# Kernel optimization log

Measured on AMD Instinct MI355X. Metric: run time of the kernel, lower is better.

## Reference

```python
import jax, jax.numpy as jnp
import numpy as np

R = 32            # voxel resolution
DIM = 240         # channels C
EPS_NORM = 0.0    # module eps
BN_EPS = 1e-5     # torch BatchNorm1d default eps


def setup_inputs() -> dict:
    key = jax.random.key(0)
    k1, k2, k3 = jax.random.split(key, 3)
    B, C, N = 4, DIM, 32768
    features = jax.random.normal(k1, (B, C, N), jnp.float32)
    coords = jax.random.uniform(k2, (B, 3, N), jnp.float32)
    # mlp params: Conv1d(2C -> C, kernel 1) + BatchNorm1d(C)
    w = jax.random.normal(k3, (C, 2 * C), jnp.float32) / np.sqrt(2 * C).astype(np.float32)
    b = jnp.zeros((C,), jnp.float32)
    gamma = jnp.ones((C,), jnp.float32)
    beta = jnp.zeros((C,), jnp.float32)
    return {"features": features, "coords": coords, "w": w, "b": b, "gamma": gamma, "beta": beta}


def _voxelize(features, coords):
    # normalize coords into [0, 1], scale to voxel grid
    nc = coords - coords.mean(axis=2, keepdims=True)                      # [B,3,N]
    scale = jnp.linalg.norm(nc, axis=1, keepdims=True).max(axis=2, keepdims=True) * 2.0 + EPS_NORM
    nc = nc / scale + 0.5
    nc = jnp.clip(nc * R, 0, R - 1)
    vox = jnp.round(nc).astype(jnp.int32)
    pos = vox[:, 0] + vox[:, 1] * R + vox[:, 2] * (R * R)                 # [B,N] flattened voxel id
    R3 = R * R * R

    def per_batch(f, p):
        # f: [C,N], p: [N] -> [2C, R3]; per-voxel max feature + second (min) feature
        mx = jax.ops.segment_max(f.T, p, num_segments=R3)                 # [R3, C]
        mn = jax.ops.segment_min(f.T, p, num_segments=R3)                 # [R3, C]
        cnt = jax.ops.segment_sum(jnp.ones_like(p), p, num_segments=R3)  # [R3]
        mask = (cnt > 0)[:, None]
        mx = jnp.where(mask, mx, 0.0)
        mn = jnp.where(mask, mn, 0.0)
        return jnp.concatenate([mx, mn], axis=1).T                        # [2C, R3]

    fea = jax.vmap(per_batch)(features, pos)                              # [B,2C,R3]
    return fea, nc


def reference(features, coords, w, b, gamma, beta):
    fea, nc = _voxelize(features, coords)
    # 1x1 Conv1d (pointwise GEMM) + BatchNorm1d (training-mode batch stats) + Swish
    y = jnp.einsum('co,bov->bcv', w, fea) + b[None, :, None]
    mean = y.mean(axis=(0, 2), keepdims=True)
    var = y.var(axis=(0, 2), keepdims=True)
    y = gamma[None, :, None] * (y - mean) * jax.lax.rsqrt(var + BN_EPS) + beta[None, :, None]
    y = y * jax.nn.sigmoid(y)
    B, C, _ = features.shape
    return y.reshape(B, C, R, R, R), nc
```

## Files before the change

kernel.cpp:

```cpp
#include <hip/hip_runtime.h>
#include <cstdint>
#include <cstddef>

#define RR 32
#define R3 32768
#define NPT 32768
#define CH 240
#define CH2 480
#define NB 4
#define NTILES 2048
#define Y_ELEMS 31457280

typedef __attribute__((ext_vector_type(8))) short short8v;
typedef __attribute__((ext_vector_type(4))) float float4v;

union u8pack { short8v v; unsigned short u[8]; };

static __device__ __forceinline__ float bf2f(unsigned short u) {
  return __uint_as_float(((unsigned int)u) << 16);
}
static __device__ __forceinline__ unsigned short f2bf(float f) {
  unsigned int u = __float_as_uint(f);
  u = (u + 0x7FFFu + ((u >> 16) & 1u)) >> 16;
  return (unsigned short)u;
}

__global__ void k_init(int* __restrict__ cnt, float* __restrict__ stats,
                       const float* __restrict__ w, unsigned short* __restrict__ wfrag,
                       int* __restrict__ tilectr) {
  int g = blockIdx.x * 256 + threadIdx.x;
  if (g == 0) *tilectr = 0;
  if (g < NB * R3) cnt[g] = 0;
  if (g < 4096) stats[g] = 0.0f;
  if (g < 14400) {
    int lane = g & 63, t = g >> 6;
    int mg = t / 75, r = t % 75;
    int kc = r / 5, mL = r % 5;
    int m = mg * 5 + mL;
    int ln = lane & 15, q = lane >> 4;
    const float* src = w + (size_t)(m * 16 + ln) * CH2 + kc * 32 + q * 8;
    u8pack pk;
#pragma unroll
    for (int j = 0; j < 8; j++) pk.u[j] = f2bf(src[j]);
    *(short8v*)&wfrag[(size_t)g * 8] = pk.v;
  }
}

__global__ __launch_bounds__(1024) void k_coord_stats(const float* __restrict__ coords,
                                                      float* __restrict__ ms) {
  __shared__ float red[1024];
  __shared__ float mean[3];
  int b = blockIdx.x, t = threadIdx.x;
  const float4* cb4 = (const float4*)(coords + (size_t)b * 3 * NPT);
  float s[3] = {0.f, 0.f, 0.f};
  for (int i = t; i < NPT / 4; i += 1024) {
#pragma unroll
    for (int d = 0; d < 3; d++) {
      float4 v = cb4[d * (NPT / 4) + i];
      s[d] += (v.x + v.y) + (v.z + v.w);
    }
  }
  for (int d = 0; d < 3; d++) {
    red[t] = s[d]; __syncthreads();
    for (int k = 512; k > 0; k >>= 1) { if (t < k) red[t] += red[t + k]; __syncthreads(); }
    if (t == 0) mean[d] = red[0] * (1.0f / NPT);
    __syncthreads();
  }
  float m0 = mean[0], m1 = mean[1], m2 = mean[2];
  float mx = 0.f;
  for (int i = t; i < NPT / 4; i += 1024) {
    float4 x = cb4[i], y = cb4[NPT / 4 + i], z = cb4[2 * (NPT / 4) + i];
    float dx, dy, dz, n;
    dx = x.x - m0; dy = y.x - m1; dz = z.x - m2; n = dx * dx + dy * dy + dz * dz; mx = fmaxf(mx, n);
    dx = x.y - m0; dy = y.y - m1; dz = z.y - m2; n = dx * dx + dy * dy + dz * dz; mx = fmaxf(mx, n);
    dx = x.z - m0; dy = y.z - m1; dz = z.z - m2; n = dx * dx + dy * dy + dz * dz; mx = fmaxf(mx, n);
    dx = x.w - m0; dy = y.w - m1; dz = z.w - m2; n = dx * dx + dy * dy + dz * dz; mx = fmaxf(mx, n);
  }
  red[t] = mx; __syncthreads();
  for (int k = 512; k > 0; k >>= 1) { if (t < k) red[t] = fmaxf(red[t], red[t + k]); __syncthreads(); }
  if (t == 0) {
    ms[b * 4 + 0] = m0; ms[b * 4 + 1] = m1; ms[b * 4 + 2] = m2;
    ms[b * 4 + 3] = sqrtf(red[0]) * 2.0f;
  }
}

__global__ void k_pos_nc(const float* __restrict__ coords, const float* __restrict__ ms,
                         float* __restrict__ ncout, int* __restrict__ pos, int* __restrict__ cnt) {
  int g = blockIdx.x * 256 + threadIdx.x;
  int b = g >> 15, i = g & (NPT - 1);
  const float* cb = coords + (size_t)b * 3 * NPT;
  float scale = ms[b * 4 + 3];
  int vox[3];
#pragma unroll
  for (int d = 0; d < 3; d++) {
    float v = (cb[(size_t)d * NPT + i] - ms[b * 4 + d]) / scale + 0.5f;
    v = fminf(fmaxf(v * (float)RR, 0.0f), (float)(RR - 1));
    ncout[((size_t)(b * 3 + d)) * NPT + i] = v;
    vox[d] = (int)rintf(v);
  }
  int p = (b << 15) | (vox[0] + (vox[1] << 5) + (vox[2] << 10));
  pos[g] = p;
  atomicAdd(&cnt[p], 1);
}

__global__ void k_scan(const int* __restrict__ cnt, int* __restrict__ offs) {
  __shared__ int part[1024];
  int b = blockIdx.x, t = threadIdx.x;
  const int base = b * R3;
  int local[32];
  int s = 0;
#pragma unroll
  for (int j = 0; j < 32; j++) { local[j] = cnt[base + t * 32 + j]; s += local[j]; }
  part[t] = s; __syncthreads();
  for (int d = 1; d < 1024; d <<= 1) {
    int v = (t >= d) ? part[t - d] : 0;
    __syncthreads();
    part[t] += v;
    __syncthreads();
  }
  int run = (t == 0) ? 0 : part[t - 1];
#pragma unroll
  for (int j = 0; j < 32; j++) { offs[base + t * 32 + j] = run; run += local[j]; }
}

__global__ void k_scatter(const int* __restrict__ pos, int* __restrict__ offs,
                          int* __restrict__ rank) {
  int g = blockIdx.x * 256 + threadIdx.x;
  int p = pos[g];
  int slot = atomicAdd(&offs[p], 1);
  rank[g] = slot;
}

__global__ void k_transpose3(const float* __restrict__ f, const int* __restrict__ rank,
                             unsigned short* __restrict__ fts) {
  __shared__ float tile[CH * 65];
  __shared__ int slts[64];
  int p0 = blockIdx.x * 64, b = blockIdx.y;
  int t = threadIdx.x;
  if (t < 64) slts[t] = rank[b * NPT + p0 + t];
  {
    int pp = t & 63, cq = t >> 6;
    const float* src = f + ((size_t)b * CH) * NPT + p0 + pp;
#pragma unroll 4
    for (int j = 0; j < 60; ++j) {
      int c = j * 4 + cq;
      tile[c * 65 + pp] = src[(size_t)c * NPT];
    }
  }
  __syncthreads();
  int ch8 = t & 7;
#pragma unroll
  for (int pass = 0; pass < 2; ++pass) {
    int p = pass * 32 + (t >> 3);
    unsigned short* dst = fts + ((size_t)(b * NPT + slts[p])) * CH;
#pragma unroll
    for (int i = 0; i < 4; ++i) {
      int ch = ch8 + 8 * i;
      if (ch < 30) {
        u8pack pk;
#pragma unroll
        for (int jj = 0; jj < 8; ++jj) pk.u[jj] = f2bf(tile[(ch * 8 + jj) * 65 + p]);
        *(short8v*)&dst[ch * 8] = pk.v;
      }
    }
  }
}

__global__ __launch_bounds__(512, 4) void k_fused(const int* __restrict__ cnt,
                                                  const int* __restrict__ offs,
                                                  const unsigned short* __restrict__ fts,
                                                  const unsigned short* __restrict__ wfrag,
                                                  const float* __restrict__ bias,
                                                  unsigned short* __restrict__ ybf,
                                                  float* __restrict__ gstats,
                                                  int* __restrict__ tilectr) {
  __shared__ unsigned short fB[4 * 15 * 512];
  __shared__ int scnt[64], soffs[64], vlist[64];
  __shared__ int qh, qm, tilebuf[2];
  int tid = threadIdx.x;
  int wave = tid >> 6, lane = tid & 63;
  int sub = lane >> 5, l = lane & 31;
  int ln = lane & 15, q = lane >> 4;

  int t1c = 30 + l;
  int kc0 = l >> 2, q0 = l & 3;
  int kc1 = t1c >> 2, q1 = t1c & 3;

  int nmt = (wave == 7) ? 1 : 2;
  int mt0 = wave * 2, mt1 = wave * 2 + (nmt - 1);
  const unsigned short* wp0 = wfrag + ((size_t)((mt0 / 5) * 75 + (mt0 % 5)) * 512) + lane * 8;
  const unsigned short* wp1 = wfrag + ((size_t)((mt1 / 5) * 75 + (mt1 % 5)) * 512) + lane * 8;

  float bb[2][4];
#pragma unroll
  for (int mm = 0; mm < 2; ++mm) {
    int mt = (mm == 0) ? mt0 : mt1;
#pragma unroll
    for (int r = 0; r < 4; ++r) bb[mm][r] = bias[mt * 16 + q * 4 + r];
  }
  float sacc[2][4], sqacc[2][4];
#pragma unroll
  for (int mm = 0; mm < 2; ++mm)
#pragma unroll
    for (int r = 0; r < 4; ++r) { sacc[mm][r] = 0.f; sqacc[mm][r] = 0.f; }

  int par = 0;
  if (tid == 0) tilebuf[0] = atomicAdd(tilectr, 1);

  while (true) {
    __syncthreads();
    int T = tilebuf[par];
    if (T >= NTILES) break;
    int b = T >> 9;
    int bbase = b << 15;
    int v0 = (T & 511) * 64;

    {
      int4 z4 = {0, 0, 0, 0};
      for (int i = tid; i < 3840; i += 512) ((int4*)fB)[i] = z4;
    }
    if (wave == 0) {
      int n = cnt[T * 64 + lane];
      int st = offs[T * 64 + lane];
      scnt[lane] = n; soffs[lane] = st;
      unsigned long long mask = __ballot(n > 0);
      int pfx = __popcll(mask & ((1ull << lane) - 1ull));
      if (n > 0) vlist[pfx] = lane;
      if (lane == 0) { qm = __popcll(mask); qh = 0; }
    }
    if (tid == 0) tilebuf[par ^ 1] = atomicAdd(tilectr, 1);
    par ^= 1;
    __syncthreads();

    int qmL = qm;
    while (true) {
      int p;
      if (l == 0) p = atomicAdd(&qh, 1);
      p = __shfl(p, sub << 5);
      if (p >= qmL) break;
      int lv = vlist[p];
      int n = scnt[lv];
      int start = soffs[lv] - n;
      int cg = lv >> 4, cc = lv & 15;
      if (l < 30) {
        const unsigned short* sp = fts + (size_t)(bbase + start) * CH + l * 8;
        int lim = (n - 1) * CH;
        float mx[8], mn[8];
#pragma unroll
        for (int k = 0; k < 8; k++) { mx[k] = -__builtin_inff(); mn[k] = __builtin_inff(); }
        for (int j = 0; j < n; j += 8) {
          int base = j * CH;
          u8pack u0, u1, u2, u3, u4, u5, u6, u7;
          int o0 = base;           o0 = o0 < lim ? o0 : lim;
          int o1 = base + CH;      o1 = o1 < lim ? o1 : lim;
          int o2 = base + 2 * CH;  o2 = o2 < lim ? o2 : lim;
          int o3 = base + 3 * CH;  o3 = o3 < lim ? o3 : lim;
          int o4 = base + 4 * CH;  o4 = o4 < lim ? o4 : lim;
          int o5 = base + 5 * CH;  o5 = o5 < lim ? o5 : lim;
          int o6 = base + 6 * CH;  o6 = o6 < lim ? o6 : lim;
          int o7 = base + 7 * CH;  o7 = o7 < lim ? o7 : lim;
          u0.v = *(const short8v*)(sp + o0);
          u1.v = *(const short8v*)(sp + o1);
          u2.v = *(const short8v*)(sp + o2);
          u3.v = *(const short8v*)(sp + o3);
          u4.v = *(const short8v*)(sp + o4);
          u5.v = *(const short8v*)(sp + o5);
          u6.v = *(const short8v*)(sp + o6);
          u7.v = *(const short8v*)(sp + o7);
#pragma unroll
          for (int k = 0; k < 8; k++) {
            float a0 = bf2f(u0.u[k]), a1 = bf2f(u1.u[k]);
            float a2 = bf2f(u2.u[k]), a3 = bf2f(u3.u[k]);
            float a4 = bf2f(u4.u[k]), a5 = bf2f(u5.u[k]);
            float a6 = bf2f(u6.u[k]), a7 = bf2f(u7.u[k]);
            float hx = fmaxf(fmaxf(fmaxf(a0, a1), fmaxf(a2, a3)),
                             fmaxf(fmaxf(a4, a5), fmaxf(a6, a7)));
            float hn = fminf(fminf(fminf(a0, a1), fminf(a2, a3)),
                             fminf(fminf(a4, a5), fminf(a6, a7)));
            mx[k] = fmaxf(mx[k], hx);
            mn[k] = fminf(mn[k], hn);
          }
        }
        u8pack omx, omn;
#pragma unroll
        for (int k = 0; k < 8; k++) { omx.u[k] = f2bf(mx[k]); omn.u[k] = f2bf(mn[k]); }
        int ci0 = (q0 * 16 + cc) ^ (kc0 & 7);
        int ci1 = (q1 * 16 + cc) ^ (kc1 & 7);
        *(short8v*)&fB[((cg * 15 + kc0) * 64 + ci0) * 8] = omx.v;
        *(short8v*)&fB[((cg * 15 + kc1) * 64 + ci1) * 8] = omn.v;
      }
    }
    __syncthreads();

    float4v acc[2][4];
#pragma unroll
    for (int mm = 0; mm < 2; ++mm)
#pragma unroll
      for (int cg = 0; cg < 4; ++cg) acc[mm][cg] = (float4v){0.f, 0.f, 0.f, 0.f};

    short8v w0[2], w1[2];
    w0[0] = *(const short8v*)(wp0);
    w0[1] = *(const short8v*)(wp0 + 5 * 512);
    w1[0] = *(const short8v*)(wp1);
    w1[1] = *(const short8v*)(wp1 + 5 * 512);
#pragma unroll
    for (int kc = 0; kc < 15; ++kc) {
      const unsigned short* fbl = fB + (size_t)((lane ^ (kc & 7)) * 8);
      short8v bfv[4];
#pragma unroll
      for (int cg = 0; cg < 4; ++cg)
        bfv[cg] = *(const short8v*)(fbl + (size_t)(cg * 15 + kc) * 512);
      short8v wn0, wn1;
      if (kc + 2 < 15) {
        wn0 = *(const short8v*)(wp0 + (size_t)(kc + 2) * 5 * 512);
        wn1 = *(const short8v*)(wp1 + (size_t)(kc + 2) * 5 * 512);
      }
#pragma unroll
      for (int cg = 0; cg < 4; ++cg)
        acc[0][cg] = __builtin_amdgcn_mfma_f32_16x16x32_bf16(w0[kc & 1], bfv[cg], acc[0][cg], 0, 0, 0);
      if (nmt > 1)
#pragma unroll
        for (int cg = 0; cg < 4; ++cg)
          acc[1][cg] = __builtin_amdgcn_mfma_f32_16x16x32_bf16(w1[kc & 1], bfv[cg], acc[1][cg], 0, 0, 0);
      if (kc + 2 < 15) { w0[kc & 1] = wn0; w1[kc & 1] = wn1; }
    }

    unsigned short* yb = ybf + ((size_t)b * CH) * R3 + v0 + ln;
#pragma unroll
    for (int mm = 0; mm < 2; ++mm)
      if (mm < nmt) {
        int mt = (mm == 0) ? mt0 : mt1;
#pragma unroll
        for (int r = 0; r < 4; ++r) {
          int c = mt * 16 + q * 4 + r;
          unsigned short* yrow = yb + (size_t)c * R3;
          float bbv = bb[mm][r];
          float s = 0.f, sq = 0.f;
#pragma unroll
          for (int cg = 0; cg < 4; ++cg) {
            float yv = acc[mm][cg][r] + bbv;
            yrow[cg * 16] = f2bf(yv);
            s += yv; sq += yv * yv;
          }
          sacc[mm][r] += s;
          sqacc[mm][r] += sq;
        }
      }
  }

  float* gslot = gstats + (size_t)(blockIdx.x & 7) * 512;
#pragma unroll
  for (int mm = 0; mm < 2; ++mm)
    if (mm < nmt) {
      int mt = (mm == 0) ? mt0 : mt1;
#pragma unroll
      for (int r = 0; r < 4; ++r) {
        float s = sacc[mm][r], sq = sqacc[mm][r];
#pragma unroll
        for (int off = 1; off < 16; off <<= 1) {
          s += __shfl_xor(s, off);
          sq += __shfl_xor(sq, off);
        }
        if (ln == 0) {
          int c = mt * 16 + q * 4 + r;
          atomicAdd(&gslot[c], s);
          atomicAdd(&gslot[256 + c], sq);
        }
      }
    }
}

__global__ void k_apply(const unsigned short* __restrict__ ybf, float* __restrict__ out,
                        const float* __restrict__ stats, const float* __restrict__ gamma,
                        const float* __restrict__ beta) {
  int g = blockIdx.x * 256 + threadIdx.x;
  int c = (g >> 12) % CH;
  const float ninv = 1.0f / (float)(NB * R3);
  float sum = 0.f, ssq = 0.f;
#pragma unroll
  for (int sl = 0; sl < 8; ++sl) {
    sum += stats[sl * 512 + c];
    ssq += stats[sl * 512 + 256 + c];
  }
  float mean = sum * ninv;
  float var = ssq * ninv - mean * mean;
  float s = gamma[c] * rsqrtf(var + 1e-5f);
  float h = beta[c] - mean * s;
  u8pack v;
  v.v = *(const short8v*)(ybf + (size_t)g * 8);
  float4 o0, o1;
  float t;
  t = bf2f(v.u[0]) * s + h; o0.x = t / (1.0f + __expf(-t));
  t = bf2f(v.u[1]) * s + h; o0.y = t / (1.0f + __expf(-t));
  t = bf2f(v.u[2]) * s + h; o0.z = t / (1.0f + __expf(-t));
  t = bf2f(v.u[3]) * s + h; o0.w = t / (1.0f + __expf(-t));
  t = bf2f(v.u[4]) * s + h; o1.x = t / (1.0f + __expf(-t));
  t = bf2f(v.u[5]) * s + h; o1.y = t / (1.0f + __expf(-t));
  t = bf2f(v.u[6]) * s + h; o1.z = t / (1.0f + __expf(-t));
  t = bf2f(v.u[7]) * s + h; o1.w = t / (1.0f + __expf(-t));
  ((float4*)out)[(size_t)g * 2] = o0;
  ((float4*)out)[(size_t)g * 2 + 1] = o1;
}

extern "C" void kernel_launch(void* const* d_in, const int* in_sizes, int n_in,
                              void* d_out, int out_size, void* d_ws, size_t ws_size,
                              hipStream_t stream) {
  const float* features = (const float*)d_in[0];
  const float* coords   = (const float*)d_in[1];
  const float* w        = (const float*)d_in[2];
  const float* bias     = (const float*)d_in[3];
  const float* gamma    = (const float*)d_in[4];
  const float* beta     = (const float*)d_in[5];
  float* out = (float*)d_out;

  char* ws = (char*)d_ws;
  size_t off = 0;
  float* ms    = (float*)(ws + off); off += 256;
  int* tilectr = (int*)(ws + off);   off += 256;
  float* stats = (float*)(ws + off); off += 16384;
  int* pos     = (int*)(ws + off);   off += (size_t)NB * NPT * 4;
  int* cnt     = (int*)(ws + off);   off += (size_t)NB * R3 * 4;
  int* offs    = (int*)(ws + off);   off += (size_t)NB * R3 * 4;
  int* rank    = (int*)(ws + off);   off += (size_t)NB * NPT * 4;
  unsigned short* wfrag = (unsigned short*)(ws + off); off += (size_t)CH * CH2 * 2;
  unsigned short* fts   = (unsigned short*)(ws + off); off += (size_t)NB * NPT * CH * 2;
  unsigned short* ybf   = (unsigned short*)(ws + off); off += (size_t)NB * R3 * CH * 2;

  float* ncout = out + Y_ELEMS;

  k_init<<<516, 256, 0, stream>>>(cnt, stats, w, wfrag, tilectr);
  k_coord_stats<<<4, 1024, 0, stream>>>(coords, ms);
  k_pos_nc<<<512, 256, 0, stream>>>(coords, ms, ncout, pos, cnt);
  k_scan<<<4, 1024, 0, stream>>>(cnt, offs);
  k_scatter<<<512, 256, 0, stream>>>(pos, offs, rank);
  k_transpose3<<<dim3(512, 4), 256, 0, stream>>>(features, rank, fts);
  k_fused<<<512, 512, 0, stream>>>(cnt, offs, fts, wfrag, bias, ybf, stats, tilectr);
  k_apply<<<Y_ELEMS / 2048, 256, 0, stream>>>(ybf, out, stats, gamma, beta);
}
```

Baseline: 430.1 us.

## Software-pipeline voxel gather with MFMA GEMM using double-buffered LDS tiles

Measured after the change: 364.6 us. 1.18x faster.

```diff
diff --git a/kernel.cpp b/kernel.cpp
--- a/kernel.cpp
+++ b/kernel.cpp
@@ -166,7 +166,7 @@
   }
 }
 
-__global__ __launch_bounds__(512, 4) void k_fused(const int* __restrict__ cnt,
+__global__ __launch_bounds__(512, 2) void k_fused(const int* __restrict__ cnt,
                                                   const int* __restrict__ offs,
                                                   const unsigned short* __restrict__ fts,
                                                   const unsigned short* __restrict__ wfrag,
@@ -174,73 +174,57 @@
                                                   unsigned short* __restrict__ ybf,
                                                   float* __restrict__ gstats,
                                                   int* __restrict__ tilectr) {
-  __shared__ unsigned short fB[4 * 15 * 512];
-  __shared__ int scnt[64], soffs[64], vlist[64];
-  __shared__ int qh, qm, tilebuf[2];
+  __shared__ unsigned short fB[2][4 * 15 * 512];
+  __shared__ int scnt[2][64], soffs[2][64], vlist[2][64];
+  __shared__ int qh[2], qm[2], tq[4];
   int tid = threadIdx.x;
   int wave = tid >> 6, lane = tid & 63;
   int sub = lane >> 5, l = lane & 31;
   int ln = lane & 15, q = lane >> 4;
 
+  int nmt = (wave == 7) ? 1 : 2;
+  short8v wreg[2][15];
+#pragma unroll
+  for (int mm = 0; mm < 2; ++mm)
+    if (mm < nmt) {
+      int mt = wave * 2 + mm;
+      int mg = mt / 5, mL = mt % 5;
+      const unsigned short* wp = wfrag + ((size_t)(mg * 75 + mL) * 512) + lane * 8;
+#pragma unroll
+      for (int kc = 0; kc < 15; ++kc)
+        wreg[mm][kc] = *(const short8v*)(wp + (size_t)kc * 5 * 512);
+    }
+
+  float bb[2][4];
+#pragma unroll
+  for (int mm = 0; mm < 2; ++mm)
+    if (mm < nmt) {
+      int mt = wave * 2 + mm;
+#pragma unroll
+      for (int r = 0; r < 4; ++r) bb[mm][r] = bias[mt * 16 + q * 4 + r];
+    }
+  float sacc[2][4], sqacc[2][4];
+#pragma unroll
+  for (int mm = 0; mm < 2; ++mm)
+#pragma unroll
+    for (int r = 0; r < 4; ++r) { sacc[mm][r] = 0.f; sqacc[mm][r] = 0.f; }
+
   int t1c = 30 + l;
   int kc0 = l >> 2, q0 = l & 3;
   int kc1 = t1c >> 2, q1 = t1c & 3;
 
-  int nmt = (wave == 7) ? 1 : 2;
-  int mt0 = wave * 2, mt1 = wave * 2 + (nmt - 1);
-  const unsigned short* wp0 = wfrag + ((size_t)((mt0 / 5) * 75 + (mt0 % 5)) * 512) + lane * 8;
-  const unsigned short* wp1 = wfrag + ((size_t)((mt1 / 5) * 75 + (mt1 % 5)) * 512) + lane * 8;
-
-  float bb[2][4];
-#pragma unroll
-  for (int mm = 0; mm < 2; ++mm) {
-    int mt = (mm == 0) ? mt0 : mt1;
-#pragma unroll
-    for (int r = 0; r < 4; ++r) bb[mm][r] = bias[mt * 16 + q * 4 + r];
-  }
-  float sacc[2][4], sqacc[2][4];
-#pragma unroll
-  for (int mm = 0; mm < 2; ++mm)
-#pragma unroll
-    for (int r = 0; r < 4; ++r) { sacc[mm][r] = 0.f; sqacc[mm][r] = 0.f; }
-
-  int par = 0;
-  if (tid == 0) tilebuf[0] = atomicAdd(tilectr, 1);
-
-  while (true) {
-    __syncthreads();
-    int T = tilebuf[par];
-    if (T >= NTILES) break;
-    int b = T >> 9;
-    int bbase = b << 15;
-    int v0 = (T & 511) * 64;
-
-    {
-      int4 z4 = {0, 0, 0, 0};
-      for (int i = tid; i < 3840; i += 512) ((int4*)fB)[i] = z4;
-    }
-    if (wave == 0) {
-      int n = cnt[T * 64 + lane];
-      int st = offs[T * 64 + lane];
-      scnt[lane] = n; soffs[lane] = st;
-      unsigned long long mask = __ballot(n > 0);
-      int pfx = __popcll(mask & ((1ull << lane) - 1ull));
-      if (n > 0) vlist[pfx] = lane;
-      if (lane == 0) { qm = __popcll(mask); qh = 0; }
-    }
-    if (tid == 0) tilebuf[par ^ 1] = atomicAdd(tilectr, 1);
-    par ^= 1;
-    __syncthreads();
-
-    int qmL = qm;
+  auto GATHER = [&](int sb, int T) {
+    unsigned short* fb = fB[sb];
+    int bbase = (T >> 9) << 15;
+    int qmL = qm[sb];
     while (true) {
       int p;
-      if (l == 0) p = atomicAdd(&qh, 1);
+      if (l == 0) p = atomicAdd(&qh[sb], 1);
       p = __shfl(p, sub << 5);
       if (p >= qmL) break;
-      int lv = vlist[p];
-      int n = scnt[lv];
-      int start = soffs[lv] - n;
+      int lv = vlist[sb][p];
+      int n = scnt[sb][lv];
+      int start = soffs[sb][lv] - n;
       int cg = lv >> 4, cc = lv & 15;
       if (l < 30) {
         const unsigned short* sp = fts + (size_t)(bbase + start) * CH + l * 8;
@@ -286,11 +270,69 @@
         for (int k = 0; k < 8; k++) { omx.u[k] = f2bf(mx[k]); omn.u[k] = f2bf(mn[k]); }
         int ci0 = (q0 * 16 + cc) ^ (kc0 & 7);
         int ci1 = (q1 * 16 + cc) ^ (kc1 & 7);
-        *(short8v*)&fB[((cg * 15 + kc0) * 64 + ci0) * 8] = omx.v;
-        *(short8v*)&fB[((cg * 15 + kc1) * 64 + ci1) * 8] = omn.v;
+        *(short8v*)&fb[((cg * 15 + kc0) * 64 + ci0) * 8] = omx.v;
+        *(short8v*)&fb[((cg * 15 + kc1) * 64 + ci1) * 8] = omn.v;
       }
     }
+  };
+
+  if (wave == 0) {
+    int t;
+    if (lane == 0) t = atomicAdd(tilectr, 1);
+    int T0w = __shfl(t, 0);
+    if (lane == 0) t = atomicAdd(tilectr, 1);
+    int T1w = __shfl(t, 0);
+    if (lane == 0) { tq[0] = T0w; tq[1] = T1w; }
+    int na = 0, oa = 0, nb2 = 0, ob = 0;
+    if (T0w < NTILES) { na = cnt[T0w * 64 + lane]; oa = offs[T0w * 64 + lane]; }
+    if (T1w < NTILES) { nb2 = cnt[T1w * 64 + lane]; ob = offs[T1w * 64 + lane]; }
+    scnt[0][lane] = na; soffs[0][lane] = oa;
+    {
+      unsigned long long m = __ballot(na > 0);
+      int pfx = __popcll(m & ((1ull << lane) - 1ull));
+      if (na > 0) vlist[0][pfx] = lane;
+      if (lane == 0) { qm[0] = __popcll(m); qh[0] = 0; }
+    }
+    scnt[1][lane] = nb2; soffs[1][lane] = ob;
+    {
+      unsigned long long m = __ballot(nb2 > 0);
+      int pfx = __popcll(m & ((1ull << lane) - 1ull));
+      if (nb2 > 0) vlist[1][pfx] = lane;
+      if (lane == 0) { qm[1] = __popcll(m); qh[1] = 0; }
+    }
+  }
+  {
+    int4 z4 = {0, 0, 0, 0};
+    for (int i2 = tid; i2 < 3840; i2 += 512) ((int4*)fB[0])[i2] = z4;
+  }
+  __syncthreads();
+  {
+    int T0v = tq[0];
+    if (T0v < NTILES) GATHER(0, T0v);
+  }
+
+  for (int it = 0;; ++it) {
     __syncthreads();
+    int T = tq[it & 3];
+    if (T >= NTILES) break;
+    int cb = it & 1, nb = cb ^ 1;
+    int Tn = tq[(it + 1) & 3];
+
+    {
+      int4 z4 = {0, 0, 0, 0};
+      for (int i2 = tid; i2 < 3840; i2 += 512) ((int4*)fB[nb])[i2] = z4;
+    }
+    int n2 = 0, o2 = 0;
+    if (wave == 0) {
+      int t;
+      if (lane == 0) t = atomicAdd(tilectr, 1);
+      int Tn2 = __shfl(t, 0);
+      if (lane == 0) tq[(it + 2) & 3] = Tn2;
+      if (Tn2 < NTILES) { n2 = cnt[Tn2 * 64 + lane]; o2 = offs[Tn2 * 64 + lane]; }
+    }
+    __syncthreads();
+
+    if (Tn < NTILES) GATHER(nb, Tn);
 
     float4v acc[2][4];
 #pragma unroll
@@ -298,38 +340,29 @@
 #pragma unroll
       for (int cg = 0; cg < 4; ++cg) acc[mm][cg] = (float4v){0.f, 0.f, 0.f, 0.f};
 
-    short8v w0[2], w1[2];
-    w0[0] = *(const short8v*)(wp0);
-    w0[1] = *(const short8v*)(wp0 + 5 * 512);
-    w1[0] = *(const short8v*)(wp1);
-    w1[1] = *(const short8v*)(wp1 + 5 * 512);
+    const unsigned short* fbase = fB[cb];
 #pragma unroll
     for (int kc = 0; kc < 15; ++kc) {
-      const unsigned short* fbl = fB + (size_t)((lane ^ (kc & 7)) * 8);
+      const unsigned short* fbl = fbase + (size_t)((lane ^ (kc & 7)) * 8);
       short8v bfv[4];
 #pragma unroll
       for (int cg = 0; cg < 4; ++cg)
         bfv[cg] = *(const short8v*)(fbl + (size_t)(cg * 15 + kc) * 512);
-      short8v wn0, wn1;
-      if (kc + 2 < 15) {
-        wn0 = *(const short8v*)(wp0 + (size_t)(kc + 2) * 5 * 512);
-        wn1 = *(const short8v*)(wp1 + (size_t)(kc + 2) * 5 * 512);
-      }
-#pragma unroll
-      for (int cg = 0; cg < 4; ++cg)
-        acc[0][cg] = __builtin_amdgcn_mfma_f32_16x16x32_bf16(w0[kc & 1], bfv[cg], acc[0][cg], 0, 0, 0);
-      if (nmt > 1)
-#pragma unroll
-        for (int cg = 0; cg < 4; ++cg)
-          acc[1][cg] = __builtin_amdgcn_mfma_f32_16x16x32_bf16(w1[kc & 1], bfv[cg], acc[1][cg], 0, 0, 0);
-      if (kc + 2 < 15) { w0[kc & 1] = wn0; w1[kc & 1] = wn1; }
-    }
-
-    unsigned short* yb = ybf + ((size_t)b * CH) * R3 + v0 + ln;
+#pragma unroll
+      for (int mm = 0; mm < 2; ++mm)
+        if (mm < nmt)
+#pragma unroll
+          for (int cg = 0; cg < 4; ++cg)
+            acc[mm][cg] = __builtin_amdgcn_mfma_f32_16x16x32_bf16(wreg[mm][kc], bfv[cg], acc[mm][cg], 0, 0, 0);
+    }
+
+    int bt = T >> 9;
+    int v0 = (T & 511) * 64;
+    unsigned short* yb = ybf + ((size_t)bt * CH) * R3 + v0 + ln;
 #pragma unroll
     for (int mm = 0; mm < 2; ++mm)
       if (mm < nmt) {
-        int mt = (mm == 0) ? mt0 : mt1;
+        int mt = wave * 2 + mm;
 #pragma unroll
         for (int r = 0; r < 4; ++r) {
           int c = mt * 16 + q * 4 + r;
@@ -346,13 +379,22 @@
           sqacc[mm][r] += sq;
         }
       }
+
+    if (wave == 0) {
+      int s2 = it & 1;
+      scnt[s2][lane] = n2; soffs[s2][lane] = o2;
+      unsigned long long m = __ballot(n2 > 0);
+      int pfx = __popcll(m & ((1ull << lane) - 1ull));
+      if (n2 > 0) vlist[s2][pfx] = lane;
+      if (lane == 0) { qm[s2] = __popcll(m); qh[s2] = 0; }
+    }
   }
 
   float* gslot = gstats + (size_t)(blockIdx.x & 7) * 512;
 #pragma unroll
   for (int mm = 0; mm < 2; ++mm)
     if (mm < nmt) {
-      int mt = (mm == 0) ? mt0 : mt1;
+      int mt = wave * 2 + mm;
 #pragma unroll
       for (int r = 0; r < 4; ++r) {
         float s = sacc[mm][r], sq = sqacc[mm][r];
@@ -434,6 +476,6 @@
   k_scan<<<4, 1024, 0, stream>>>(cnt, offs);
   k_scatter<<<512, 256, 0, stream>>>(pos, offs, rank);
   k_transpose3<<<dim3(512, 4), 256, 0, stream>>>(features, rank, fts);
-  k_fused<<<512, 512, 0, stream>>>(cnt, offs, fts, wfrag, bias, ybf, stats, tilectr);
+  k_fused<<<256, 512, 0, stream>>>(cnt, offs, fts, wfrag, bias, ybf, stats, tilectr);
   k_apply<<<Y_ELEMS / 2048, 256, 0, stream>>>(ybf, out, stats, gamma, beta);
 }
```
